# Optimization experiments

Hardware: AMD Instinct MI355X
Metric: run time of the kernel (lower is better)

Reference implementation:

```python
import jax, jax.numpy as jnp
import numpy as np

NUM_EXPERTS = 8
TOP_K = 2
B, S, H = 4, 1024, 1024
FF = 2 * H  # expert hidden = 2*hidden_size per the torch code


def setup_inputs() -> dict:
    key = jax.random.key(0)
    ks = jax.random.split(key, 5)
    scale = 0.02
    return {
        "x": jax.random.normal(ks[0], (B, S, H), dtype=jnp.float32),
        "Wg": jax.random.normal(ks[1], (H, NUM_EXPERTS), dtype=jnp.float32) * scale,
        "bg": jnp.zeros((NUM_EXPERTS,), dtype=jnp.float32),
        "W1": jax.random.normal(ks[2], (NUM_EXPERTS, H, FF), dtype=jnp.float32) * scale,
        "b1": jnp.zeros((NUM_EXPERTS, FF), dtype=jnp.float32),
        "W2": jax.random.normal(ks[3], (NUM_EXPERTS, FF, H), dtype=jnp.float32) * scale,
        "b2": jnp.zeros((NUM_EXPERTS, H), dtype=jnp.float32),
    }


def reference(x, Wg, bg, W1, b1, W2, b2):
    b, s, h = x.shape
    xf = x.reshape(-1, h)  # [T, H]
    # Gating: softmax over experts, then top-k and renormalize (as in torch code)
    gate_scores = jax.nn.softmax(xf @ Wg + bg, axis=-1)  # [T, E]
    top_v, top_i = jax.lax.top_k(gate_scores, TOP_K)      # [T, K]
    top_v = top_v / jnp.sum(top_v, axis=-1, keepdims=True)
    # Combine weights per (token, expert): gate if expert selected else 0
    combine = jnp.sum(jax.nn.one_hot(top_i, NUM_EXPERTS, dtype=xf.dtype)
                      * top_v[..., None], axis=1)         # [T, E]
    # Dense all-expert MLP (eval-mode dropout = identity), then gated combine
    hmid = jax.nn.relu(jnp.einsum('th,ehf->tef', xf, W1) + b1)  # [T, E, FF]
    yexp = jnp.einsum('tef,efh->teh', hmid, W2) + b2            # [T, E, H]
    out = jnp.einsum('te,teh->th', combine, yexp)               # [T, H]
    return out.reshape(b, s, h)
```

## Files before the change

kernel.cpp:

```cpp
#include <hip/hip_runtime.h>
#include <hip/hip_bf16.h>

#define T_TOK 4096
#define HD    1024
#define FFD   2048
#define NE    8

typedef __attribute__((ext_vector_type(8))) short short8;
typedef __attribute__((ext_vector_type(4))) float f32x4;

__device__ __forceinline__ unsigned short f2bf(float f) {
  __hip_bfloat16 h = __float2bfloat16(f);
  return __builtin_bit_cast(unsigned short, h);
}

__device__ __forceinline__ void gload_lds16(const unsigned short* g, unsigned short* l) {
  __builtin_amdgcn_global_load_lds(
      (const __attribute__((address_space(1))) unsigned int*)g,
      (__attribute__((address_space(3))) unsigned int*)l, 16, 0, 0);
}

__global__ __launch_bounds__(512) void prep_kernel(
    const float* __restrict__ x, const float* __restrict__ Wg,
    const float* __restrict__ bg,
    const float* __restrict__ W1, const float* __restrict__ W2,
    int* __restrict__ top_i, float2* __restrict__ top_w,
    unsigned short* __restrict__ xbf,
    unsigned short* __restrict__ W1T, unsigned short* __restrict__ W2T,
    float* __restrict__ out)
{
  __shared__ unsigned short tt[64 * 128];
  const int bid = blockIdx.x;
  const int tid = threadIdx.x;

  if (bid < T_TOK / 8) {
    {
      size_t b = ((size_t)bid * 512 + tid) * 16;
      float4 z = make_float4(0.f, 0.f, 0.f, 0.f);
#pragma unroll
      for (int q = 0; q < 4; ++q) *(float4*)(out + b + q * 4) = z;
    }
    const int wave = tid >> 6;
    const int lane = tid & 63;
    const int t = bid * 8 + wave;

    float acc[NE];
#pragma unroll
    for (int e = 0; e < NE; ++e) acc[e] = 0.f;

    const float* xr = x + (size_t)t * HD;
    unsigned short* xo = xbf + (size_t)t * HD;
#pragma unroll
    for (int it = 0; it < 4; ++it) {
      const int h0 = lane * 4 + it * 256;
      float4 xv = *(const float4*)(xr + h0);
#pragma unroll
      for (int j = 0; j < 4; ++j) {
        float xs = (&xv.x)[j];
        float4 a = *(const float4*)(Wg + (size_t)(h0 + j) * NE);
        float4 b = *(const float4*)(Wg + (size_t)(h0 + j) * NE + 4);
        acc[0] = fmaf(xs, a.x, acc[0]); acc[1] = fmaf(xs, a.y, acc[1]);
        acc[2] = fmaf(xs, a.z, acc[2]); acc[3] = fmaf(xs, a.w, acc[3]);
        acc[4] = fmaf(xs, b.x, acc[4]); acc[5] = fmaf(xs, b.y, acc[5]);
        acc[6] = fmaf(xs, b.z, acc[6]); acc[7] = fmaf(xs, b.w, acc[7]);
      }
      ushort4 u;
      u.x = f2bf(xv.x); u.y = f2bf(xv.y); u.z = f2bf(xv.z); u.w = f2bf(xv.w);
      *(ushort4*)(xo + h0) = u;
    }
#pragma unroll
    for (int off = 32; off > 0; off >>= 1) {
#pragma unroll
      for (int e = 0; e < NE; ++e) acc[e] += __shfl_xor(acc[e], off);
    }
    if (lane == 0) {
      float lg[NE];
#pragma unroll
      for (int e = 0; e < NE; ++e) lg[e] = acc[e] + bg[e];
      int i1 = 0;
#pragma unroll
      for (int e = 1; e < NE; ++e) if (lg[e] > lg[i1]) i1 = e;
      int i2 = (i1 == 0) ? 1 : 0;
#pragma unroll
      for (int e = 0; e < NE; ++e) if (e != i1 && lg[e] > lg[i2]) i2 = e;
      float p2 = expf(lg[i2] - lg[i1]);
      float s  = 1.f + p2;
      top_i[t] = i1 | (i2 << 8);
      top_w[t] = make_float2(1.f / s, p2 / s);
    }
    return;
  }

  const float* in; unsigned short* ow; int R, C, idx;
  if (bid < T_TOK / 8 + 2048) {
    idx = bid - T_TOK / 8;          in = W1; ow = W1T; R = HD;  C = FFD;
  } else {
    idx = bid - (T_TOK / 8 + 2048); in = W2; ow = W2T; R = FFD; C = HD;
  }
  const int cpt = C >> 6;
  const int rpt = R >> 7;
  const int cx = idx % cpt;
  const int ry = (idx / cpt) % rpt;
  const int z  = idx / (cpt * rpt);
  const int r0 = ry << 7, c0 = cx << 6;

  const int rg = tid >> 4;
  const int cg = tid & 15;
  {
    const float* ip = in + ((size_t)z * R + r0 + rg * 4) * C + c0 + cg * 4;
    float4 v0 = *(const float4*)(ip);
    float4 v1 = *(const float4*)(ip + C);
    float4 v2 = *(const float4*)(ip + 2 * (size_t)C);
    float4 v3 = *(const float4*)(ip + 3 * (size_t)C);
#pragma unroll
    for (int i = 0; i < 4; ++i) {
      const int n   = cg * 4 + i;
      const int c8  = rg ^ (2 * (n & 15));
      ushort4 u;
      u.x = f2bf((&v0.x)[i]); u.y = f2bf((&v1.x)[i]);
      u.z = f2bf((&v2.x)[i]); u.w = f2bf((&v3.x)[i]);
      *(ushort4*)&tt[n * 128 + c8 * 4] = u;
    }
  }
  __syncthreads();
#pragma unroll
  for (int p = 0; p < 2; ++p) {
    const int n  = (tid >> 4) + p * 32;
    const int m  = tid & 15;
    const int c8 = (2 * m) ^ (2 * (n & 15));
    short8 val = *(const short8*)&tt[n * 128 + c8 * 4];
    *(short8*)(ow + ((size_t)z * C + c0 + n) * R + r0 + m * 8) = val;
  }
}

__global__ __launch_bounds__(256) void route_kernel(
    const int* __restrict__ top_i, const float2* __restrict__ top_w,
    int* __restrict__ counts, int* __restrict__ ids, float* __restrict__ wts)
{
  const int e   = blockIdx.x;
  const int tid = threadIdx.x;
  __shared__ int psum[256];

  const int t0 = tid * 16;
  unsigned int flags = 0;
  int cnt = 0;
#pragma unroll
  for (int j = 0; j < 16; ++j) {
    int ti = top_i[t0 + j];
    bool m = ((ti & 255) == e) || (((ti >> 8) & 255) == e);
    flags |= (m ? 1u : 0u) << j;
    cnt += m;
  }
  psum[tid] = cnt;
  __syncthreads();
  for (int off = 1; off < 256; off <<= 1) {
    int v = (tid >= off) ? psum[tid - off] : 0;
    __syncthreads();
    psum[tid] += v;
    __syncthreads();
  }
  int rank = psum[tid] - cnt;
#pragma unroll
  for (int j = 0; j < 16; ++j) {
    if (flags & (1u << j)) {
      int t = t0 + j;
      int ti = top_i[t];
      float2 w = top_w[t];
      ids[e * T_TOK + rank] = t;
      wts[e * T_TOK + rank] = ((ti & 255) == e) ? w.x : w.y;
      ++rank;
    }
  }
  if (tid == 255) counts[e] = psum[255];
}

template<int KD, int ND, bool G1M, bool GATHER_A>
__global__ __launch_bounds__(256, 4) void pair_gemm128_kernel(
    const unsigned short* __restrict__ A,
    const unsigned short* __restrict__ BT,
    const float* __restrict__ bias,
    const int* __restrict__ counts, const int* __restrict__ ids,
    const float* __restrict__ wts,
    unsigned short* __restrict__ Hout, float* __restrict__ out)
{
  constexpr int CT = ND / 128;

  const int e    = blockIdx.x & 7;
  const int slot = blockIdx.x >> 3;
  int cnt = 0, base = 0;
#pragma unroll
  for (int k = 0; k < NE; ++k) {
    int c = counts[k];
    if (k < e)  base += (c + 255) & ~255;
    if (k == e) cnt = c;
  }
  const int ntiles = (cnt + 127) >> 7;
  if (slot >= ntiles * CT) return;
  const int rt   = slot % ntiles;
  const int ct   = slot / ntiles;
  const int row0 = base + rt * 128;

  __shared__ __align__(16) unsigned short As[128 * 64];
  __shared__ __align__(16) unsigned short Bs[128 * 64];

  const int tid  = threadIdx.x;
  const int w    = tid >> 6;
  const int lane = tid & 63;
  const int g    = lane >> 4;
  const int rA   = lane & 15;
  const int wr   = w >> 1;
  const int wc   = w & 1;
  const int sw   = rA & 7;
  const int srow = lane >> 3;
  const int lc8  = ((lane & 7) ^ srow) * 8;

  const unsigned short* arow[4];
#pragma unroll
  for (int jj = 0; jj < 4; ++jj) {
    const int lrow = w * 32 + jj * 8 + srow;
    int src;
    if constexpr (GATHER_A) {
      int i = rt * 128 + lrow;
      src = ids[e * T_TOK + (i < cnt ? i : cnt - 1)];
    } else {
      src = row0 + lrow;
    }
    arow[jj] = A + (size_t)src * KD + lc8;
  }
  const unsigned short* Bb = BT + ((size_t)e * ND + (size_t)ct * 128) * KD + lc8;

  f32x4 acc[4][4];
#pragma unroll
  for (int mf = 0; mf < 4; ++mf)
#pragma unroll
    for (int nf = 0; nf < 4; ++nf)
      acc[mf][nf] = (f32x4){0.f, 0.f, 0.f, 0.f};

  for (int kc = 0; kc < KD; kc += 64) {
    __syncthreads();
#pragma unroll
    for (int jj = 0; jj < 4; ++jj) {
      const int rg = w * 32 + jj * 8;
      gload_lds16(arow[jj] + kc, &As[rg * 64]);
      gload_lds16(Bb + (size_t)(rg + srow) * KD + kc, &Bs[rg * 64]);
    }
    __syncthreads();
#pragma unroll
    for (int ks = 0; ks < 2; ++ks) {
      const int pc = ((ks * 4 + g) ^ sw) << 3;
      short8 af[4], bf[4];
#pragma unroll
      for (int mf = 0; mf < 4; ++mf)
        af[mf] = *(const short8*)&As[(wr * 64 + mf * 16 + rA) * 64 + pc];
#pragma unroll
      for (int nf = 0; nf < 4; ++nf)
        bf[nf] = *(const short8*)&Bs[(wc * 64 + nf * 16 + rA) * 64 + pc];
#pragma unroll
      for (int mf = 0; mf < 4; ++mf)
#pragma unroll
        for (int nf = 0; nf < 4; ++nf)
          acc[mf][nf] = __builtin_amdgcn_mfma_f32_16x16x32_bf16(
              af[mf], bf[nf], acc[mf][nf], 0, 0, 0);
    }
  }

  float bv[4];
#pragma unroll
  for (int nf = 0; nf < 4; ++nf)
    bv[nf] = bias[e * ND + ct * 128 + wc * 64 + nf * 16 + rA];

  if constexpr (G1M) {
#pragma unroll
    for (int mf = 0; mf < 4; ++mf)
#pragma unroll
      for (int r = 0; r < 4; ++r) {
        const int row = row0 + wr * 64 + mf * 16 + g * 4 + r;
        unsigned short* hrow = Hout + (size_t)row * FFD + ct * 128 + wc * 64 + rA;
#pragma unroll
        for (int nf = 0; nf < 4; ++nf)
          hrow[nf * 16] = f2bf(fmaxf(acc[mf][nf][r] + bv[nf], 0.f));
      }
  } else {
#pragma unroll
    for (int mf = 0; mf < 4; ++mf)
#pragma unroll
      for (int r = 0; r < 4; ++r) {
        const int i = rt * 128 + wr * 64 + mf * 16 + g * 4 + r;
        if (i >= cnt) continue;
        const int tok = ids[e * T_TOK + i];
        const float wt = wts[e * T_TOK + i];
        float* orow = out + (size_t)tok * HD + ct * 128 + wc * 64 + rA;
#pragma unroll
        for (int nf = 0; nf < 4; ++nf)
          atomicAdd(&orow[nf * 16], wt * (acc[mf][nf][r] + bv[nf]));
      }
  }
}

extern "C" void kernel_launch(void* const* d_in, const int* in_sizes, int n_in,
                              void* d_out, int out_size, void* d_ws, size_t ws_size,
                              hipStream_t stream) {
  const float* x  = (const float*)d_in[0];
  const float* Wg = (const float*)d_in[1];
  const float* bg = (const float*)d_in[2];
  const float* W1 = (const float*)d_in[3];
  const float* b1 = (const float*)d_in[4];
  const float* W2 = (const float*)d_in[5];
  const float* b2 = (const float*)d_in[6];
  float* out = (float*)d_out;

  const size_t OFF_TOPI = 512;
  const size_t OFF_TOPW = OFF_TOPI + (size_t)T_TOK * 4;
  const size_t OFF_IDS  = OFF_TOPW + (size_t)T_TOK * 8;
  const size_t OFF_WTS  = OFF_IDS + (size_t)T_TOK * NE * 4;
  const size_t OFF_XBF  = OFF_WTS + (size_t)T_TOK * NE * 4;
  const size_t OFF_W1T  = OFF_XBF + (size_t)T_TOK * HD * 2;
  const size_t OFF_W2T  = OFF_W1T + (size_t)NE * HD * FFD * 2;
  const size_t OFF_H    = OFF_W2T + (size_t)NE * HD * FFD * 2;
  const size_t REQ      = OFF_H + (size_t)10240 * FFD * 2;

  if (ws_size < REQ) return;

  int*            counts = (int*)d_ws;
  int*            top_i  = (int*)((char*)d_ws + OFF_TOPI);
  float2*         top_w  = (float2*)((char*)d_ws + OFF_TOPW);
  int*            ids    = (int*)((char*)d_ws + OFF_IDS);
  float*          wts    = (float*)((char*)d_ws + OFF_WTS);
  unsigned short* xbf    = (unsigned short*)((char*)d_ws + OFF_XBF);
  unsigned short* W1T    = (unsigned short*)((char*)d_ws + OFF_W1T);
  unsigned short* W2T    = (unsigned short*)((char*)d_ws + OFF_W2T);
  unsigned short* H      = (unsigned short*)((char*)d_ws + OFF_H);

  prep_kernel<<<T_TOK / 8 + 2 * 2048, 512, 0, stream>>>(
      x, Wg, bg, W1, W2, top_i, top_w, xbf, W1T, W2T, out);
  route_kernel<<<NE, 256, 0, stream>>>(top_i, top_w, counts, ids, wts);

  pair_gemm128_kernel<HD, FFD, true, true>
      <<<NE * 512, 256, 0, stream>>>(xbf, W1T, b1, counts, ids, wts, H, nullptr);
  pair_gemm128_kernel<FFD, HD, false, false>
      <<<NE * 256, 256, 0, stream>>>(H, W2T, b2, counts, ids, wts, nullptr, out);
}
```

Measured before the change: 169.9 us.

## Overlap W2 transpose with first expert GEMM and widen transpose tiles

Moves the fp32-to-bf16 transpose of W2 out of the prep kernel and into extra blocks appended to the first grouped GEMM launch, so that weight conversion can fill idle CUs left by early-exiting GEMM slots. The transpose routine now has each thread handle 8 rows with 16-byte LDS writes, using a new swizzle over 256-thread blocks. The prep kernel also moves to 256-thread blocks. The tradeoff is that the transpose blocks compete with GEMM blocks for bandwidth, and correctness relies on the W2T blocks finishing before the second GEMM, which stream ordering guarantees.

```diff
diff --git a/kernel.cpp b/kernel.cpp
--- a/kernel.cpp
+++ b/kernel.cpp
@@ -20,116 +20,113 @@
       (__attribute__((address_space(3))) unsigned int*)l, 16, 0, 0);
 }
 
-__global__ __launch_bounds__(512) void prep_kernel(
+__device__ __forceinline__ void transpose_tile(
+    const float* __restrict__ in, unsigned short* __restrict__ ow,
+    int R, int C, int idx, unsigned short* tt, int tid)
+{
+  const int cpt = C >> 6, rpt = R >> 7;
+  const int cx = idx % cpt;
+  const int ry = (idx / cpt) % rpt;
+  const int z  = idx / (cpt * rpt);
+  const int r0 = ry << 7, c0 = cx << 6;
+
+  const int rg  = tid >> 4;
+  const int cg  = tid & 15;
+  const int c16 = rg ^ ((cg & 3) << 2);
+
+  const float* ip = in + ((size_t)z * R + r0 + rg * 8) * C + c0 + cg * 4;
+  float4 v[8];
+#pragma unroll
+  for (int r = 0; r < 8; ++r)
+    v[r] = *(const float4*)(ip + (size_t)r * C);
+#pragma unroll
+  for (int i = 0; i < 4; ++i) {
+    const int n = cg * 4 + i;
+    short8 u;
+#pragma unroll
+    for (int r = 0; r < 8; ++r) u[r] = (short)f2bf((&v[r].x)[i]);
+    *(short8*)&tt[n * 128 + c16 * 8] = u;
+  }
+  __syncthreads();
+#pragma unroll
+  for (int p = 0; p < 4; ++p) {
+    const int n  = (tid >> 4) + p * 16;
+    const int m  = tid & 15;
+    const int rc = m ^ (((n >> 2) & 3) << 2);
+    short8 val = *(const short8*)&tt[n * 128 + rc * 8];
+    *(short8*)(ow + ((size_t)z * C + c0 + n) * R + r0 + m * 8) = val;
+  }
+}
+
+__global__ __launch_bounds__(256) void prep_kernel(
     const float* __restrict__ x, const float* __restrict__ Wg,
-    const float* __restrict__ bg,
-    const float* __restrict__ W1, const float* __restrict__ W2,
+    const float* __restrict__ bg, const float* __restrict__ W1,
     int* __restrict__ top_i, float2* __restrict__ top_w,
-    unsigned short* __restrict__ xbf,
-    unsigned short* __restrict__ W1T, unsigned short* __restrict__ W2T,
+    unsigned short* __restrict__ xbf, unsigned short* __restrict__ W1T,
     float* __restrict__ out)
 {
   __shared__ unsigned short tt[64 * 128];
   const int bid = blockIdx.x;
   const int tid = threadIdx.x;
 
-  if (bid < T_TOK / 8) {
-    {
-      size_t b = ((size_t)bid * 512 + tid) * 16;
-      float4 z = make_float4(0.f, 0.f, 0.f, 0.f);
-#pragma unroll
-      for (int q = 0; q < 4; ++q) *(float4*)(out + b + q * 4) = z;
-    }
-    const int wave = tid >> 6;
-    const int lane = tid & 63;
-    const int t = bid * 8 + wave;
-
-    float acc[NE];
-#pragma unroll
-    for (int e = 0; e < NE; ++e) acc[e] = 0.f;
-
-    const float* xr = x + (size_t)t * HD;
-    unsigned short* xo = xbf + (size_t)t * HD;
-#pragma unroll
-    for (int it = 0; it < 4; ++it) {
-      const int h0 = lane * 4 + it * 256;
-      float4 xv = *(const float4*)(xr + h0);
-#pragma unroll
-      for (int j = 0; j < 4; ++j) {
-        float xs = (&xv.x)[j];
-        float4 a = *(const float4*)(Wg + (size_t)(h0 + j) * NE);
-        float4 b = *(const float4*)(Wg + (size_t)(h0 + j) * NE + 4);
-        acc[0] = fmaf(xs, a.x, acc[0]); acc[1] = fmaf(xs, a.y, acc[1]);
-        acc[2] = fmaf(xs, a.z, acc[2]); acc[3] = fmaf(xs, a.w, acc[3]);
-        acc[4] = fmaf(xs, b.x, acc[4]); acc[5] = fmaf(xs, b.y, acc[5]);
-        acc[6] = fmaf(xs, b.z, acc[6]); acc[7] = fmaf(xs, b.w, acc[7]);
-      }
-      ushort4 u;
-      u.x = f2bf(xv.x); u.y = f2bf(xv.y); u.z = f2bf(xv.z); u.w = f2bf(xv.w);
-      *(ushort4*)(xo + h0) = u;
-    }
-#pragma unroll
-    for (int off = 32; off > 0; off >>= 1) {
-#pragma unroll
-      for (int e = 0; e < NE; ++e) acc[e] += __shfl_xor(acc[e], off);
-    }
-    if (lane == 0) {
-      float lg[NE];
-#pragma unroll
-      for (int e = 0; e < NE; ++e) lg[e] = acc[e] + bg[e];
-      int i1 = 0;
-#pragma unroll
-      for (int e = 1; e < NE; ++e) if (lg[e] > lg[i1]) i1 = e;
-      int i2 = (i1 == 0) ? 1 : 0;
-#pragma unroll
-      for (int e = 0; e < NE; ++e) if (e != i1 && lg[e] > lg[i2]) i2 = e;
-      float p2 = expf(lg[i2] - lg[i1]);
-      float s  = 1.f + p2;
-      top_i[t] = i1 | (i2 << 8);
-      top_w[t] = make_float2(1.f / s, p2 / s);
-    }
+  if (bid >= T_TOK / 4) {
+    transpose_tile(W1, W1T, HD, FFD, bid - T_TOK / 4, tt, tid);
     return;
   }
 
-  const float* in; unsigned short* ow; int R, C, idx;
-  if (bid < T_TOK / 8 + 2048) {
-    idx = bid - T_TOK / 8;          in = W1; ow = W1T; R = HD;  C = FFD;
-  } else {
-    idx = bid - (T_TOK / 8 + 2048); in = W2; ow = W2T; R = FFD; C = HD;
-  }
-  const int cpt = C >> 6;
-  const int rpt = R >> 7;
-  const int cx = idx % cpt;
-  const int ry = (idx / cpt) % rpt;
-  const int z  = idx / (cpt * rpt);
-  const int r0 = ry << 7, c0 = cx << 6;
-
-  const int rg = tid >> 4;
-  const int cg = tid & 15;
   {
-    const float* ip = in + ((size_t)z * R + r0 + rg * 4) * C + c0 + cg * 4;
-    float4 v0 = *(const float4*)(ip);
-    float4 v1 = *(const float4*)(ip + C);
-    float4 v2 = *(const float4*)(ip + 2 * (size_t)C);
-    float4 v3 = *(const float4*)(ip + 3 * (size_t)C);
-#pragma unroll
-    for (int i = 0; i < 4; ++i) {
-      const int n   = cg * 4 + i;
-      const int c8  = rg ^ (2 * (n & 15));
-      ushort4 u;
-      u.x = f2bf((&v0.x)[i]); u.y = f2bf((&v1.x)[i]);
-      u.z = f2bf((&v2.x)[i]); u.w = f2bf((&v3.x)[i]);
-      *(ushort4*)&tt[n * 128 + c8 * 4] = u;
-    }
-  }
-  __syncthreads();
-#pragma unroll
-  for (int p = 0; p < 2; ++p) {
-    const int n  = (tid >> 4) + p * 32;
-    const int m  = tid & 15;
-    const int c8 = (2 * m) ^ (2 * (n & 15));
-    short8 val = *(const short8*)&tt[n * 128 + c8 * 4];
-    *(short8*)(ow + ((size_t)z * C + c0 + n) * R + r0 + m * 8) = val;
+    size_t b = ((size_t)bid * 256 + tid) * 16;
+    float4 z = make_float4(0.f, 0.f, 0.f, 0.f);
+#pragma unroll
+    for (int q = 0; q < 4; ++q) *(float4*)(out + b + q * 4) = z;
+  }
+  const int wave = tid >> 6;
+  const int lane = tid & 63;
+  const int t = bid * 4 + wave;
+
+  float acc[NE];
+#pragma unroll
+  for (int e = 0; e < NE; ++e) acc[e] = 0.f;
+
+  const float* xr = x + (size_t)t * HD;
+  unsigned short* xo = xbf + (size_t)t * HD;
+#pragma unroll
+  for (int it = 0; it < 4; ++it) {
+    const int h0 = lane * 4 + it * 256;
+    float4 xv = *(const float4*)(xr + h0);
+#pragma unroll
+    for (int j = 0; j < 4; ++j) {
+      float xs = (&xv.x)[j];
+      float4 a = *(const float4*)(Wg + (size_t)(h0 + j) * NE);
+      float4 b = *(const float4*)(Wg + (size_t)(h0 + j) * NE + 4);
+      acc[0] = fmaf(xs, a.x, acc[0]); acc[1] = fmaf(xs, a.y, acc[1]);
+      acc[2] = fmaf(xs, a.z, acc[2]); acc[3] = fmaf(xs, a.w, acc[3]);
+      acc[4] = fmaf(xs, b.x, acc[4]); acc[5] = fmaf(xs, b.y, acc[5]);
+      acc[6] = fmaf(xs, b.z, acc[6]); acc[7] = fmaf(xs, b.w, acc[7]);
+    }
+    ushort4 u;
+    u.x = f2bf(xv.x); u.y = f2bf(xv.y); u.z = f2bf(xv.z); u.w = f2bf(xv.w);
+    *(ushort4*)(xo + h0) = u;
+  }
+#pragma unroll
+  for (int off = 32; off > 0; off >>= 1) {
+#pragma unroll
+    for (int e = 0; e < NE; ++e) acc[e] += __shfl_xor(acc[e], off);
+  }
+  if (lane == 0) {
+    float lg[NE];
+#pragma unroll
+    for (int e = 0; e < NE; ++e) lg[e] = acc[e] + bg[e];
+    int i1 = 0;
+#pragma unroll
+    for (int e = 1; e < NE; ++e) if (lg[e] > lg[i1]) i1 = e;
+    int i2 = (i1 == 0) ? 1 : 0;
+#pragma unroll
+    for (int e = 0; e < NE; ++e) if (e != i1 && lg[e] > lg[i2]) i2 = e;
+    float p2 = expf(lg[i2] - lg[i1]);
+    float s  = 1.f + p2;
+    top_i[t] = i1 | (i2 << 8);
+    top_w[t] = make_float2(1.f / s, p2 / s);
   }
 }
 
@@ -174,16 +171,30 @@
   if (tid == 255) counts[e] = psum[255];
 }
 
-template<int KD, int ND, bool G1M, bool GATHER_A>
+template<int KD, int ND, bool G1M, bool GATHER_A, bool FUSET>
 __global__ __launch_bounds__(256, 4) void pair_gemm128_kernel(
     const unsigned short* __restrict__ A,
     const unsigned short* __restrict__ BT,
     const float* __restrict__ bias,
     const int* __restrict__ counts, const int* __restrict__ ids,
     const float* __restrict__ wts,
-    unsigned short* __restrict__ Hout, float* __restrict__ out)
+    unsigned short* __restrict__ Hout, float* __restrict__ out,
+    const float* __restrict__ Wsrc, unsigned short* __restrict__ Wdst,
+    int TR, int TC, int tbase)
 {
   constexpr int CT = ND / 128;
+
+  __shared__ __align__(16) unsigned short As[128 * 64];
+  __shared__ __align__(16) unsigned short Bs[128 * 64];
+
+  const int tid = threadIdx.x;
+
+  if constexpr (FUSET) {
+    if ((int)blockIdx.x >= tbase) {
+      transpose_tile(Wsrc, Wdst, TR, TC, blockIdx.x - tbase, As, tid);
+      return;
+    }
+  }
 
   const int e    = blockIdx.x & 7;
   const int slot = blockIdx.x >> 3;
@@ -200,10 +211,6 @@
   const int ct   = slot / ntiles;
   const int row0 = base + rt * 128;
 
-  __shared__ __align__(16) unsigned short As[128 * 64];
-  __shared__ __align__(16) unsigned short Bs[128 * 64];
-
-  const int tid  = threadIdx.x;
   const int w    = tid >> 6;
   const int lane = tid & 63;
   const int g    = lane >> 4;
@@ -331,12 +338,15 @@
   unsigned short* W2T    = (unsigned short*)((char*)d_ws + OFF_W2T);
   unsigned short* H      = (unsigned short*)((char*)d_ws + OFF_H);
 
-  prep_kernel<<<T_TOK / 8 + 2 * 2048, 512, 0, stream>>>(
-      x, Wg, bg, W1, W2, top_i, top_w, xbf, W1T, W2T, out);
+  prep_kernel<<<T_TOK / 4 + 2048, 256, 0, stream>>>(
+      x, Wg, bg, W1, top_i, top_w, xbf, W1T, out);
   route_kernel<<<NE, 256, 0, stream>>>(top_i, top_w, counts, ids, wts);
 
-  pair_gemm128_kernel<HD, FFD, true, true>
-      <<<NE * 512, 256, 0, stream>>>(xbf, W1T, b1, counts, ids, wts, H, nullptr);
-  pair_gemm128_kernel<FFD, HD, false, false>
-      <<<NE * 256, 256, 0, stream>>>(H, W2T, b2, counts, ids, wts, nullptr, out);
-}
+  const int tbase = NE * 512;
+  pair_gemm128_kernel<HD, FFD, true, true, true>
+      <<<tbase + 2048, 256, 0, stream>>>(xbf, W1T, b1, counts, ids, wts, H, nullptr,
+                                         W2, W2T, FFD, HD, tbase);
+  pair_gemm128_kernel<FFD, HD, false, false, false>
+      <<<NE * 256, 256, 0, stream>>>(H, W2T, b2, counts, ids, wts, nullptr, out,
+                                     nullptr, nullptr, 0, 0, 0);
+}
```

After: 167.4 us. Within noise of the previous version (-1.5%).
